# Optimization experiments

Measured on AMD Instinct MI355X. Metric: run time of the kernel, lower is better.

The kernel has to match this reference:

```python
import jax, jax.numpy as jnp
import numpy as np

NUM_HEADS = 16
HEAD_DIM = 128
HIDDEN = NUM_HEADS * HEAD_DIM


def rotate_half(x):
    x1, x2 = jnp.split(x, 2, axis=-1)
    return jnp.concatenate((-x2, x1), axis=-1)


def setup_inputs() -> dict:
    key = jax.random.key(0)
    ks = jax.random.split(key, 7)
    b, s = 2, 2048
    return {
        "hidden_states": jax.random.normal(ks[0], (b, s, HIDDEN), dtype=jnp.float32),
        "cos": jax.random.normal(ks[1], (1, 1, s, HEAD_DIM), dtype=jnp.float32),
        "sin": jax.random.normal(ks[2], (1, 1, s, HEAD_DIM), dtype=jnp.float32),
        "Wq": jax.random.normal(ks[3], (HIDDEN, HIDDEN), dtype=jnp.float32) * 0.02,
        "Wk": jax.random.normal(ks[4], (HIDDEN, HIDDEN), dtype=jnp.float32) * 0.02,
        "Wv": jax.random.normal(ks[5], (HIDDEN, HIDDEN), dtype=jnp.float32) * 0.02,
        "Wo": jax.random.normal(ks[6], (HIDDEN, HIDDEN), dtype=jnp.float32) * 0.02,
    }


def reference(hidden_states, cos, sin, Wq, Wk, Wv, Wo):
    b, s, _ = hidden_states.shape

    def proj(W):
        # [b,s,hidden] -> [b,H,s,D]
        return (hidden_states @ W).reshape(b, s, NUM_HEADS, HEAD_DIM).transpose(0, 2, 1, 3)

    q = proj(Wq)
    k = proj(Wk)
    v = proj(Wv)

    # RoPE: cos/sin [1,1,s,D] broadcast over batch and heads
    q = q * cos + rotate_half(q) * sin
    k = k * cos + rotate_half(k) * sin

    scale = 1.0 / jnp.sqrt(jnp.asarray(HEAD_DIM, dtype=q.dtype))
    scores = jnp.einsum("bhqd,bhkd->bhqk", q, k) * scale  # [b,H,s,s]
    attn = jax.nn.softmax(scores, axis=-1)  # no mask applied (matches source)
    out = jnp.einsum("bhqk,bhkd->bhqd", attn, v)  # [b,H,s,D]
    out = out.transpose(0, 2, 1, 3).reshape(b, s, HIDDEN)
    return out @ Wo
```

## Files before the change

kernel.cpp:

```cpp
#include <hip/hip_runtime.h>

typedef short bf16x8 __attribute__((ext_vector_type(8)));
typedef float f32x4 __attribute__((ext_vector_type(4)));

#define HID   2048
#define S_LEN 2048
#define NH    16
#define HD    128
#define BATCH 2
#define NROWS (BATCH * S_LEN)

__device__ __forceinline__ float bf2f(unsigned short u) {
    union { unsigned int i; float f; } v;
    v.i = ((unsigned int)u) << 16;
    return v.f;
}
__device__ __forceinline__ unsigned short f2bf(float f) {
    union { float f; unsigned int i; } v;
    v.f = f;
    unsigned int u = v.i;
    return (unsigned short)((u + 0x7fffu + ((u >> 16) & 1u)) >> 16);
}

__device__ __forceinline__ unsigned int pkbf(float a, float b) {
#if defined(__has_builtin) && __has_builtin(__builtin_amdgcn_cvt_pk_bf16_f32)
    typedef __bf16 bf2_t __attribute__((ext_vector_type(2)));
    bf2_t v = __builtin_amdgcn_cvt_pk_bf16_f32(a, b);
    unsigned int u;
    __builtin_memcpy(&u, &v, 4);
    return u;
#else
    return (unsigned int)f2bf(a) | ((unsigned int)f2bf(b) << 16);
#endif
}

__device__ __forceinline__ float exp2_fast(float x) {
#if defined(__has_builtin) && __has_builtin(__builtin_amdgcn_exp2f)
    return __builtin_amdgcn_exp2f(x);
#else
    return __expf(x * 0.6931471805599453f);
#endif
}

__device__ __forceinline__ void async16(const unsigned short* g, unsigned short* l) {
    __builtin_amdgcn_global_load_lds(
        (const __attribute__((address_space(1))) unsigned int*)g,
        (__attribute__((address_space(3))) unsigned int*)l, 16, 0, 0);
}

__global__ __launch_bounds__(256) void prep(const float* __restrict__ hs,
                                            const float* __restrict__ Wa,
                                            const float* __restrict__ Wb,
                                            const float* __restrict__ Wc,
                                            unsigned short* __restrict__ Xb,
                                            unsigned short* __restrict__ WT) {
    int z = blockIdx.z;
    int t = threadIdx.x;
    if (z == 3) {
        size_t idx = (((size_t)blockIdx.y * 64 + blockIdx.x) * 256 + t) * 8;
        float4 v0 = *(const float4*)(hs + idx);
        float4 v1 = *(const float4*)(hs + idx + 4);
        uint4 o;
        o.x = pkbf(v0.x, v0.y);
        o.y = pkbf(v0.z, v0.w);
        o.z = pkbf(v1.x, v1.y);
        o.w = pkbf(v1.z, v1.w);
        *(uint4*)(Xb + idx) = o;
        return;
    }
    __shared__ float tile[32][33];
    int tx = t & 31, ty = t >> 5;
    int bx = blockIdx.x, by = blockIdx.y;
    const float* W = (z == 0) ? Wa : ((z == 1) ? Wb : Wc);
    unsigned short* dst = WT + (size_t)z * HID * HID;
#pragma unroll
    for (int i = 0; i < 4; i++)
        tile[ty + i * 8][tx] = W[(size_t)(by * 32 + ty + i * 8) * HID + bx * 32 + tx];
    __syncthreads();
#pragma unroll
    for (int i = 0; i < 4; i++)
        dst[(size_t)(bx * 32 + ty + i * 8) * HID + by * 32 + tx] = f2bf(tile[tx][ty + i * 8]);
}

__global__ __launch_bounds__(256) void transpose_cast(const float* __restrict__ W,
                                                      unsigned short* __restrict__ WT) {
    __shared__ float tile[32][33];
    int t = threadIdx.x;
    int tx = t & 31, ty = t >> 5;
    int bx = blockIdx.x, by = blockIdx.y;
#pragma unroll
    for (int i = 0; i < 4; i++)
        tile[ty + i * 8][tx] = W[(size_t)(by * 32 + ty + i * 8) * HID + bx * 32 + tx];
    __syncthreads();
#pragma unroll
    for (int i = 0; i < 4; i++)
        WT[(size_t)(bx * 32 + ty + i * 8) * HID + by * 32 + tx] = f2bf(tile[tx][ty + i * 8]);
}

__global__ __launch_bounds__(512, 2) void gemm_qkv(const unsigned short* __restrict__ A,
                                                   const unsigned short* __restrict__ Bt,
                                                   unsigned short* __restrict__ Qo,
                                                   unsigned short* __restrict__ Ko,
                                                   unsigned short* __restrict__ Vo,
                                                   const float* __restrict__ cosp,
                                                   const float* __restrict__ sinp) {
    __shared__ unsigned short SM[49152];
    int t = threadIdx.x;
    int w = t >> 6, lane = t & 63;
    int wm = w >> 2, wn = w & 3;
    int c = lane & 15, quad = lane >> 4;

    int bid = blockIdx.x;
    int wgid = (bid & 7) * 64 + (bid >> 3);
    int bx = wgid >> 5, by = wgid & 31;
    int m0 = by * 128, n0 = bx * 384;

    int srow = lane >> 2;
    int schk = (lane & 3) ^ ((lane >> 3) & 3);
    const unsigned short* Agp = A  + (size_t)(m0 + w * 16 + srow) * HID + schk * 8;
    const unsigned short* Bgp = Bt + (size_t)(n0 + w * 16 + srow) * HID + schk * 8;

    f32x4 zero = {0.f, 0.f, 0.f, 0.f};
    f32x4 acc[4][6];
#pragma unroll
    for (int i = 0; i < 4; i++)
#pragma unroll
        for (int j = 0; j < 6; j++) acc[i][j] = zero;

#pragma unroll
    for (int p = 0; p < 2; p++) {
        unsigned short* S = SM + p * 16384;
        async16(Agp + p * 32, S + w * 512);
#pragma unroll
        for (int j = 0; j < 3; j++)
            async16(Bgp + p * 32 + (size_t)j * 128 * HID, S + 4096 + j * 4096 + w * 512);
    }
    __builtin_amdgcn_s_waitcnt(0x0F74);
    __builtin_amdgcn_s_barrier();

    int rofs = (quad ^ ((c >> 1) & 3)) * 8;

    int scur = 0;
    for (int kt = 0; kt < 64; kt++) {
        const unsigned short* Sa = SM + scur * 16384;
        const unsigned short* Sb = Sa + 4096;
        int ktn = kt + 2; if (ktn > 63) ktn = 63;
        int snx = scur + 2; if (snx >= 3) snx -= 3;
        unsigned short* Sn = SM + snx * 16384;

        async16(Agp + ktn * 32, Sn + w * 512);
        bf16x8 af[2], bfr[6];
#pragma unroll
        for (int mt = 0; mt < 2; mt++)
            af[mt] = *(const bf16x8*)(Sa + (wm * 64 + mt * 16 + c) * 32 + rofs);
#pragma unroll
        for (int nt = 0; nt < 6; nt++)
            bfr[nt] = *(const bf16x8*)(Sb + (wn * 96 + nt * 16 + c) * 32 + rofs);
        __builtin_amdgcn_s_barrier();
        __builtin_amdgcn_s_setprio(1);
#pragma unroll
        for (int mt = 0; mt < 2; mt++)
#pragma unroll
            for (int nt = 0; nt < 6; nt++)
                acc[mt][nt] = __builtin_amdgcn_mfma_f32_16x16x32_bf16(af[mt], bfr[nt],
                                                                      acc[mt][nt], 0, 0, 0);
        __builtin_amdgcn_s_setprio(0);
        __builtin_amdgcn_s_barrier();

#pragma unroll
        for (int j = 0; j < 3; j++)
            async16(Bgp + ktn * 32 + (size_t)j * 128 * HID, Sn + 4096 + j * 4096 + w * 512);
        bf16x8 ag[2];
#pragma unroll
        for (int mt = 0; mt < 2; mt++)
            ag[mt] = *(const bf16x8*)(Sa + (wm * 64 + (mt + 2) * 16 + c) * 32 + rofs);
        __builtin_amdgcn_s_waitcnt(0x0F74);
        __builtin_amdgcn_s_barrier();
        __builtin_amdgcn_s_setprio(1);
#pragma unroll
        for (int mt = 0; mt < 2; mt++)
#pragma unroll
            for (int nt = 0; nt < 6; nt++)
                acc[mt + 2][nt] = __builtin_amdgcn_mfma_f32_16x16x32_bf16(ag[mt], bfr[nt],
                                                                          acc[mt + 2][nt], 0, 0, 0);
        __builtin_amdgcn_s_setprio(0);
        __builtin_amdgcn_s_barrier();

        scur = (scur + 1 == 3) ? 0 : scur + 1;
    }

    __syncthreads();

#pragma unroll
    for (int mt = 0; mt < 4; mt++) {
#pragma unroll
        for (int nt = 0; nt < 6; nt++) {
            ushort4 o;
            o.x = f2bf(acc[mt][nt][0]);
            o.y = f2bf(acc[mt][nt][1]);
            o.z = f2bf(acc[mt][nt][2]);
            o.w = f2bf(acc[mt][nt][3]);
            *(ushort4*)(SM + (w * 6 + nt) * 256 + lane * 4) = o;
        }
        __syncthreads();
#pragma unroll
        for (int nt = 0; nt < 6; nt++) {
            int colbase = n0 + wn * 96 + nt * 16;
            int mat = colbase >> 11;
            int h = (colbase & 2047) >> 7;
            int dc = (colbase & 127) + c;
            if (mat == 2) {
                int row0 = m0 + wm * 64 + mt * 16 + quad * 4;
                int b = row0 >> 11, s = row0 & 2047;
                ushort4 o;
                o.x = f2bf(acc[mt][nt][0]);
                o.y = f2bf(acc[mt][nt][1]);
                o.z = f2bf(acc[mt][nt][2]);
                o.w = f2bf(acc[mt][nt][3]);
                *(ushort4*)(Vo + ((size_t)(b * NH + h) * HD + dc) * S_LEN + s) = o;
            } else {
                int q2 = (wn * 96 + nt * 16) ^ 64;
                int wn2 = q2 / 96;
                int nt2 = (q2 - wn2 * 96) >> 4;
                ushort4 pv = *(const ushort4*)(SM + ((wm * 4 + wn2) * 6 + nt2) * 256 + lane * 4);
                float part[4] = {bf2f(pv.x), bf2f(pv.y), bf2f(pv.z), bf2f(pv.w)};
                float sgn = ((colbase >> 6) & 1) ? 1.0f : -1.0f;
                unsigned short* Cb = (mat == 0) ? Qo : Ko;
                float scl = (mat == 0) ? 0.12751743f : 1.0f;
#pragma unroll
                for (int r = 0; r < 4; r++) {
                    int row = m0 + wm * 64 + mt * 16 + quad * 4 + r;
                    int b = row >> 11, s = row & 2047;
                    float cv = cosp[s * HD + dc], sv = sinp[s * HD + dc];
                    float out = (acc[mt][nt][r] * cv + sgn * part[r] * sv) * scl;
                    Cb[((size_t)(b * NH + h) * S_LEN + s) * HD + dc] = f2bf(out);
                }
            }
        }
        __syncthreads();
    }
}

template <int MODE>
__global__ __launch_bounds__(256, 2) void gemm_bt(const unsigned short* __restrict__ A,
                                                  const unsigned short* __restrict__ Bt,
                                                  unsigned short* __restrict__ Qo,
                                                  unsigned short* __restrict__ Ko,
                                                  unsigned short* __restrict__ Vo,
                                                  float* __restrict__ Fo,
                                                  const float* __restrict__ cosp,
                                                  const float* __restrict__ sinp,
                                                  int n_shift) {
    __shared__ unsigned short SM[16384];
    unsigned short* Asm = SM;
    unsigned short* Bsm = SM + 8192;
    int t = threadIdx.x;
    int wave = t >> 6, lane = t & 63;
    int wm = wave >> 1, wn = wave & 1;
    int c = lane & 15, quad = lane >> 4;
    int m0 = blockIdx.y * 128, nloc = blockIdx.x * 128;

    int lr = lane >> 3;
    int cb = (lane & 7) ^ (lr & 7);
    const unsigned short* Ag = A + (size_t)(m0 + wave * 32 + lr) * HID + cb * 8;
    const unsigned short* Bg = Bt + (size_t)(nloc + wave * 32 + lr) * HID + cb * 8;
    unsigned short* Al = Asm + wave * 2048;
    unsigned short* Bl = Bsm + wave * 2048;

    f32x4 zero = {0.f, 0.f, 0.f, 0.f};
    f32x4 acc[4][4];
#pragma unroll
    for (int i = 0; i < 4; i++)
#pragma unroll
        for (int j = 0; j < 4; j++) acc[i][j] = zero;

    for (int it = 0; it < 32; it++) {
        int k0 = it * 64;
#pragma unroll
        for (int j = 0; j < 4; j++) {
            async16(Ag + k0 + j * 8 * HID, Al + j * 512);
            async16(Bg + k0 + j * 8 * HID, Bl + j * 512);
        }
        __syncthreads();
#pragma unroll
        for (int kk = 0; kk < 2; kk++) {
            bf16x8 af[4], bfr[4];
#pragma unroll
            for (int mt = 0; mt < 4; mt++)
                af[mt] = *(const bf16x8*)(Asm + (wm * 64 + mt * 16 + c) * 64 +
                                          (((kk * 4 + quad) ^ (c & 7)) * 8));
#pragma unroll
            for (int nt = 0; nt < 4; nt++)
                bfr[nt] = *(const bf16x8*)(Bsm + (wn * 64 + nt * 16 + c) * 64 +
                                           (((kk * 4 + quad) ^ (c & 7)) * 8));
#pragma unroll
            for (int mt = 0; mt < 4; mt++)
#pragma unroll
                for (int nt = 0; nt < 4; nt++)
                    acc[mt][nt] = __builtin_amdgcn_mfma_f32_16x16x32_bf16(af[mt], bfr[nt],
                                                                          acc[mt][nt], 0, 0, 0);
        }
        __syncthreads();
    }

    if (MODE == 2) {
#pragma unroll
        for (int mt = 0; mt < 4; mt++)
#pragma unroll
            for (int nt = 0; nt < 4; nt++)
#pragma unroll
                for (int r = 0; r < 4; r++) {
                    int row = m0 + wm * 64 + mt * 16 + quad * 4 + r;
                    int col = nloc + wn * 64 + nt * 16 + c;
                    Fo[(size_t)row * HID + col] = acc[mt][nt][r];
                }
    } else {
        int nglob0 = n_shift + nloc;
        int mat = nglob0 >> 11;
        int h = (nglob0 & 2047) >> 7;
        if (mat == 2) {
#pragma unroll
            for (int mt = 0; mt < 4; mt++)
#pragma unroll
                for (int nt = 0; nt < 4; nt++) {
                    int d = wn * 64 + nt * 16 + c;
                    int row0 = m0 + wm * 64 + mt * 16 + quad * 4;
                    int b = row0 >> 11, s = row0 & 2047;
                    ushort4 o;
                    o.x = f2bf(acc[mt][nt][0]);
                    o.y = f2bf(acc[mt][nt][1]);
                    o.z = f2bf(acc[mt][nt][2]);
                    o.w = f2bf(acc[mt][nt][3]);
                    *(ushort4*)(Vo + ((size_t)(b * NH + h) * HD + d) * S_LEN + s) = o;
                }
        } else {
            unsigned short* Cb = (mat == 0) ? Qo : Ko;
            float scl = (mat == 0) ? 0.12751743f : 1.0f;
            __syncthreads();
#pragma unroll
            for (int mt = 0; mt < 4; mt++)
#pragma unroll
                for (int nt = 0; nt < 4; nt++) {
                    ushort4 o;
                    o.x = f2bf(acc[mt][nt][0]);
                    o.y = f2bf(acc[mt][nt][1]);
                    o.z = f2bf(acc[mt][nt][2]);
                    o.w = f2bf(acc[mt][nt][3]);
                    *(ushort4*)(SM + (mt * 4 + nt) * 1024 + t * 4) = o;
                }
            __syncthreads();
            int partner = (wm * 2 + (wn ^ 1)) * 64 + lane;
            float sgn = wn ? 1.0f : -1.0f;
#pragma unroll
            for (int mt = 0; mt < 4; mt++) {
#pragma unroll
                for (int nt = 0; nt < 4; nt++) {
                    ushort4 pv = *(const ushort4*)(SM + (mt * 4 + nt) * 1024 + partner * 4);
                    float part[4] = {bf2f(pv.x), bf2f(pv.y), bf2f(pv.z), bf2f(pv.w)};
                    int col = wn * 64 + nt * 16 + c;
#pragma unroll
                    for (int r = 0; r < 4; r++) {
                        int row = m0 + wm * 64 + mt * 16 + quad * 4 + r;
                        int b = row >> 11, s = row & 2047;
                        float cv = cosp[s * HD + col], sv = sinp[s * HD + col];
                        float out = (acc[mt][nt][r] * cv + sgn * part[r] * sv) * scl;
                        Cb[((size_t)(b * NH + h) * S_LEN + s) * HD + col] = f2bf(out);
                    }
                }
            }
        }
    }
}

#define PKS 72
__global__ __launch_bounds__(256, 2) void attn_kernel(const unsigned short* __restrict__ Q,
                                                      const unsigned short* __restrict__ Kg,
                                                      const unsigned short* __restrict__ Vt,
                                                      unsigned short* __restrict__ Aout) {
    __shared__ unsigned short Ksm[64 * 128];
    __shared__ unsigned short Vsm[128 * 64];
    __shared__ __align__(16) unsigned short Psm[4 * 2 * 16 * PKS];
    int bh = blockIdx.y;
    int b = bh >> 4, h = bh & 15;
    int t = threadIdx.x;
    int wave = t >> 6, lane = t & 63;
    int c = lane & 15, quad = lane >> 4;
    int q0 = blockIdx.x * 128 + wave * 32;
    const unsigned short* Qp = Q + (size_t)bh * S_LEN * HD;
    const unsigned short* Kp = Kg + (size_t)bh * S_LEN * HD;
    const unsigned short* Vp = Vt + (size_t)bh * HD * S_LEN;

    bf16x8 qf[2][4];
#pragma unroll
    for (int qn = 0; qn < 2; qn++)
#pragma unroll
        for (int kk = 0; kk < 4; kk++)
            qf[qn][kk] = *(const bf16x8*)(Qp + (size_t)(q0 + qn * 16 + c) * HD + kk * 32 + quad * 8);

    f32x4 zero = {0.f, 0.f, 0.f, 0.f};
    f32x4 o_acc[2][8];
#pragma unroll
    for (int qn = 0; qn < 2; qn++)
#pragma unroll
        for (int nt = 0; nt < 8; nt++) o_acc[qn][nt] = zero;
    float lsum[2] = {0.f, 0.f};

    for (int key0 = 0; key0 < S_LEN; key0 += 64) {
#pragma unroll
        for (int j = 0; j < 4; j++) {
            int fc = (wave * 4 + j) * 64 + lane;
            int rK = fc >> 4, cbK = (fc & 15) ^ (rK & 15);
            async16(Kp + (size_t)(key0 + rK) * HD + cbK * 8, Ksm + (wave * 4 + j) * 512);
            int rV = fc >> 3, cbV = (fc & 7) ^ (rV & 7);
            async16(Vp + (size_t)rV * S_LEN + key0 + cbV * 8, Vsm + (wave * 4 + j) * 512);
        }
        __syncthreads();

        f32x4 sacc[4][2];
#pragma unroll
        for (int km = 0; km < 4; km++)
#pragma unroll
            for (int qn = 0; qn < 2; qn++) sacc[km][qn] = zero;
#pragma unroll
        for (int kk = 0; kk < 4; kk++) {
            bf16x8 kfr[4];
#pragma unroll
            for (int km = 0; km < 4; km++)
                kfr[km] = *(const bf16x8*)(Ksm + (km * 16 + c) * HD + (((kk * 4 + quad) ^ c)) * 8);
#pragma unroll
            for (int km = 0; km < 4; km++)
#pragma unroll
                for (int qn = 0; qn < 2; qn++)
                    sacc[km][qn] = __builtin_amdgcn_mfma_f32_16x16x32_bf16(kfr[km], qf[qn][kk],
                                                                           sacc[km][qn], 0, 0, 0);
        }

#pragma unroll
        for (int qn = 0; qn < 2; qn++) {
#pragma unroll
            for (int km = 0; km < 4; km++) {
                float e0 = exp2_fast(sacc[km][qn][0]);
                float e1 = exp2_fast(sacc[km][qn][1]);
                float e2 = exp2_fast(sacc[km][qn][2]);
                float e3 = exp2_fast(sacc[km][qn][3]);
                lsum[qn] += (e0 + e1) + (e2 + e3);
                uint2 pk;
                pk.x = pkbf(e0, e1);
                pk.y = pkbf(e2, e3);
                *(uint2*)(Psm + ((wave * 2 + qn) * 16 + c) * PKS + km * 16 + quad * 4) = pk;
            }
        }
        asm volatile("" ::: "memory");
        __builtin_amdgcn_s_waitcnt(0xc07f);
        asm volatile("" ::: "memory");

#pragma unroll
        for (int kf = 0; kf < 2; kf++) {
            bf16x8 pf[2];
#pragma unroll
            for (int qn = 0; qn < 2; qn++)
                pf[qn] = *(const bf16x8*)(Psm + ((wave * 2 + qn) * 16 + c) * PKS + kf * 32 + quad * 8);
#pragma unroll
            for (int nt = 0; nt < 8; nt++) {
                bf16x8 vf = *(const bf16x8*)(Vsm + (nt * 16 + c) * 64 +
                                             (((kf * 4 + quad) ^ (c & 7))) * 8);
#pragma unroll
                for (int qn = 0; qn < 2; qn++)
                    o_acc[qn][nt] = __builtin_amdgcn_mfma_f32_16x16x32_bf16(pf[qn], vf,
                                                                            o_acc[qn][nt], 0, 0, 0);
            }
        }
        __syncthreads();
    }

#pragma unroll
    for (int qn = 0; qn < 2; qn++) {
        lsum[qn] += __shfl_xor(lsum[qn], 16);
        lsum[qn] += __shfl_xor(lsum[qn], 32);
    }
    float inv[2][4];
#pragma unroll
    for (int qn = 0; qn < 2; qn++)
#pragma unroll
        for (int r = 0; r < 4; r++)
            inv[qn][r] = 1.0f / __shfl(lsum[qn], quad * 4 + r);

#pragma unroll
    for (int qn = 0; qn < 2; qn++) {
#pragma unroll
        for (int r = 0; r < 4; r++) {
            int srow = q0 + qn * 16 + quad * 4 + r;
            size_t base = ((size_t)(b * S_LEN + srow)) * HID + h * HD;
#pragma unroll
            for (int nt = 0; nt < 8; nt++)
                Aout[base + nt * 16 + c] = f2bf(o_acc[qn][nt][r] * inv[qn][r]);
        }
    }
}

extern "C" void kernel_launch(void* const* d_in, const int* in_sizes, int n_in,
                              void* d_out, int out_size, void* d_ws, size_t ws_size,
                              hipStream_t stream) {
    const float* hs   = (const float*)d_in[0];
    const float* cosp = (const float*)d_in[1];
    const float* sinp = (const float*)d_in[2];
    const float* Wq   = (const float*)d_in[3];
    const float* Wk   = (const float*)d_in[4];
    const float* Wv   = (const float*)d_in[5];
    const float* Wo   = (const float*)d_in[6];

    char* ws = (char*)d_ws;
    unsigned short* Xb = (unsigned short*)(ws);
    unsigned short* Qb = (unsigned short*)(ws + (16ull << 20));
    unsigned short* Kb = (unsigned short*)(ws + (32ull << 20));
    unsigned short* Vb = (unsigned short*)(ws + (48ull << 20));
    unsigned short* WT = (unsigned short*)(ws + (64ull << 20));

    const bool fused = ws_size >= (88ull << 20);

    if (fused) {
        prep<<<dim3(64, 64, 4), 256, 0, stream>>>(hs, Wq, Wk, Wv, Xb, WT);
        gemm_qkv<<<dim3(512), 512, 0, stream>>>(Xb, WT, Qb, Kb, Vb, cosp, sinp);
        attn_kernel<<<dim3(16, 32), 256, 0, stream>>>(Qb, Kb, Vb, Xb );
        unsigned short* WoT = (unsigned short*)(ws + (16ull << 20));
        transpose_cast<<<dim3(64, 64), 256, 0, stream>>>(Wo, WoT);
        gemm_bt<2><<<dim3(16, 32), 256, 0, stream>>>(Xb, WoT, nullptr, nullptr, nullptr,
                                                     (float*)d_out, cosp, sinp, 0);
    } else {
        prep<<<dim3(64, 64, 1), 256, 0, stream>>>(hs, Wq, Wq, Wq, Xb, WT);
        prep<<<dim3(64, 64, 4), 256, 0, stream>>>(hs, Wq, Wq, Wq, Xb, WT);
        gemm_bt<0><<<dim3(16, 32), 256, 0, stream>>>(Xb, WT, Qb, Kb, Vb, nullptr,
                                                     cosp, sinp, 0);
        transpose_cast<<<dim3(64, 64), 256, 0, stream>>>(Wk, WT);
        gemm_bt<0><<<dim3(16, 32), 256, 0, stream>>>(Xb, WT, Qb, Kb, Vb, nullptr,
                                                     cosp, sinp, 2048);
        transpose_cast<<<dim3(64, 64), 256, 0, stream>>>(Wv, WT);
        gemm_bt<0><<<dim3(16, 32), 256, 0, stream>>>(Xb, WT, Qb, Kb, Vb, nullptr,
                                                     cosp, sinp, 4096);
        attn_kernel<<<dim3(16, 32), 256, 0, stream>>>(Qb, Kb, Vb, Xb );
        transpose_cast<<<dim3(64, 64), 256, 0, stream>>>(Wo, WT);
        gemm_bt<2><<<dim3(16, 32), 256, 0, stream>>>(Xb, WT, nullptr, nullptr, nullptr,
                                                     (float*)d_out, cosp, sinp, 0);
    }
}
```

Measured before the change: 395.6 us.

## Software-pipeline QKV GEMM main loop with register double-buffered LDS fragments

Restructures the QKV projection GEMM k-loop so the next k-tile's A/B fragments are read from LDS into a second register set while the MFMAs run on the current set. The loop is unrolled by two over the three-slot LDS ring, and each k-tile now issues all of its global-to-LDS copies together. It also cuts barriers from four to one per k-tile. The cost is roughly double the fragment registers, which may lower occupancy, and a tighter reliance on slot reuse ordering for correctness.

```diff
diff --git a/kernel.cpp b/kernel.cpp
--- a/kernel.cpp
+++ b/kernel.cpp
@@ -127,66 +127,64 @@
 #pragma unroll
         for (int j = 0; j < 6; j++) acc[i][j] = zero;
 
-#pragma unroll
-    for (int p = 0; p < 2; p++) {
-        unsigned short* S = SM + p * 16384;
-        async16(Agp + p * 32, S + w * 512);
-#pragma unroll
-        for (int j = 0; j < 3; j++)
-            async16(Bgp + p * 32 + (size_t)j * 128 * HID, S + 4096 + j * 4096 + w * 512);
-    }
+#define STAGE_QKV(KTN) {                                                        \
+        unsigned short* Sn_ = SM + ((KTN) % 3) * 16384;                         \
+        async16(Agp + (KTN) * 32, Sn_ + w * 512);                               \
+        async16(Bgp + (KTN) * 32,                       Sn_ + 4096  + w * 512); \
+        async16(Bgp + (KTN) * 32 + (size_t)128 * HID,   Sn_ + 8192  + w * 512); \
+        async16(Bgp + (KTN) * 32 + (size_t)256 * HID,   Sn_ + 12288 + w * 512); }
+
+#define DSREAD_QKV(SLOT, AF, BF) {                                              \
+        const unsigned short* Sa_ = SM + (SLOT) * 16384;                        \
+        const unsigned short* Sb_ = Sa_ + 4096;                                 \
+        AF[0] = *(const bf16x8*)(Sa_ + (wm * 64 + 0 * 16 + c) * 32 + rofs);     \
+        AF[1] = *(const bf16x8*)(Sa_ + (wm * 64 + 1 * 16 + c) * 32 + rofs);     \
+        AF[2] = *(const bf16x8*)(Sa_ + (wm * 64 + 2 * 16 + c) * 32 + rofs);     \
+        AF[3] = *(const bf16x8*)(Sa_ + (wm * 64 + 3 * 16 + c) * 32 + rofs);     \
+        BF[0] = *(const bf16x8*)(Sb_ + (wn * 96 + 0 * 16 + c) * 32 + rofs);     \
+        BF[1] = *(const bf16x8*)(Sb_ + (wn * 96 + 1 * 16 + c) * 32 + rofs);     \
+        BF[2] = *(const bf16x8*)(Sb_ + (wn * 96 + 2 * 16 + c) * 32 + rofs);     \
+        BF[3] = *(const bf16x8*)(Sb_ + (wn * 96 + 3 * 16 + c) * 32 + rofs);     \
+        BF[4] = *(const bf16x8*)(Sb_ + (wn * 96 + 4 * 16 + c) * 32 + rofs);     \
+        BF[5] = *(const bf16x8*)(Sb_ + (wn * 96 + 5 * 16 + c) * 32 + rofs); }
+
+#define MFMA24(AF, BF) {                                                        \
+        _Pragma("unroll")                                                       \
+        for (int mt = 0; mt < 4; mt++)                                          \
+            _Pragma("unroll")                                                   \
+            for (int nt = 0; nt < 6; nt++)                                      \
+                acc[mt][nt] = __builtin_amdgcn_mfma_f32_16x16x32_bf16(          \
+                    AF[mt], BF[nt], acc[mt][nt], 0, 0, 0); }
+
+    STAGE_QKV(0);
+    STAGE_QKV(1);
     __builtin_amdgcn_s_waitcnt(0x0F74);
     __builtin_amdgcn_s_barrier();
 
     int rofs = (quad ^ ((c >> 1) & 3)) * 8;
-
-    int scur = 0;
-    for (int kt = 0; kt < 64; kt++) {
-        const unsigned short* Sa = SM + scur * 16384;
-        const unsigned short* Sb = Sa + 4096;
-        int ktn = kt + 2; if (ktn > 63) ktn = 63;
-        int snx = scur + 2; if (snx >= 3) snx -= 3;
-        unsigned short* Sn = SM + snx * 16384;
-
-        async16(Agp + ktn * 32, Sn + w * 512);
-        bf16x8 af[2], bfr[6];
-#pragma unroll
-        for (int mt = 0; mt < 2; mt++)
-            af[mt] = *(const bf16x8*)(Sa + (wm * 64 + mt * 16 + c) * 32 + rofs);
-#pragma unroll
-        for (int nt = 0; nt < 6; nt++)
-            bfr[nt] = *(const bf16x8*)(Sb + (wn * 96 + nt * 16 + c) * 32 + rofs);
-        __builtin_amdgcn_s_barrier();
-        __builtin_amdgcn_s_setprio(1);
-#pragma unroll
-        for (int mt = 0; mt < 2; mt++)
-#pragma unroll
-            for (int nt = 0; nt < 6; nt++)
-                acc[mt][nt] = __builtin_amdgcn_mfma_f32_16x16x32_bf16(af[mt], bfr[nt],
-                                                                      acc[mt][nt], 0, 0, 0);
-        __builtin_amdgcn_s_setprio(0);
-        __builtin_amdgcn_s_barrier();
-
-#pragma unroll
-        for (int j = 0; j < 3; j++)
-            async16(Bgp + ktn * 32 + (size_t)j * 128 * HID, Sn + 4096 + j * 4096 + w * 512);
-        bf16x8 ag[2];
-#pragma unroll
-        for (int mt = 0; mt < 2; mt++)
-            ag[mt] = *(const bf16x8*)(Sa + (wm * 64 + (mt + 2) * 16 + c) * 32 + rofs);
+    bf16x8 afA[4], bfA[6], afB[4], bfB[6];
+    DSREAD_QKV(0, afA, bfA);
+
+    for (int i = 0; i < 32; i++) {
+        int kt0 = 2 * i, kt1 = 2 * i + 1;
+        int ktn0 = kt0 + 2; if (ktn0 > 63) ktn0 = 63;
+        STAGE_QKV(ktn0);
         __builtin_amdgcn_s_waitcnt(0x0F74);
         __builtin_amdgcn_s_barrier();
+        DSREAD_QKV(kt1 % 3, afB, bfB);
+        __builtin_amdgcn_sched_barrier(0);
         __builtin_amdgcn_s_setprio(1);
-#pragma unroll
-        for (int mt = 0; mt < 2; mt++)
-#pragma unroll
-            for (int nt = 0; nt < 6; nt++)
-                acc[mt + 2][nt] = __builtin_amdgcn_mfma_f32_16x16x32_bf16(ag[mt], bfr[nt],
-                                                                          acc[mt + 2][nt], 0, 0, 0);
+        MFMA24(afA, bfA);
         __builtin_amdgcn_s_setprio(0);
+        int ktn1 = kt1 + 2; if (ktn1 > 63) ktn1 = 63;
+        STAGE_QKV(ktn1);
+        __builtin_amdgcn_s_waitcnt(0x0F74);
         __builtin_amdgcn_s_barrier();
-
-        scur = (scur + 1 == 3) ? 0 : scur + 1;
+        DSREAD_QKV((kt0 + 2) % 3, afA, bfA);
+        __builtin_amdgcn_sched_barrier(0);
+        __builtin_amdgcn_s_setprio(1);
+        MFMA24(afB, bfB);
+        __builtin_amdgcn_s_setprio(0);
     }
 
     __syncthreads();
```

Result: faster. 387.5 us (-2.1%).
